# Optimization experiments

Hardware: AMD Instinct MI355X
Metric: run time of the kernel (lower is better)

The kernel has to match this reference:

```python
import jax, jax.numpy as jnp
import numpy as np

B, S, D, H, E, K = 4, 2048, 1024, 2048, 8, 2


def setup_inputs() -> dict:
    key = jax.random.key(0)
    ks = jax.random.split(key, 5)
    x = jax.random.normal(ks[0], (B, S, D), dtype=jnp.float32)
    Wr = jax.random.normal(ks[1], (D, E), dtype=jnp.float32) * 0.02  # router weight
    w1 = jax.random.normal(ks[2], (E, D, H), dtype=jnp.float32) * 0.02  # gate proj per expert
    w3 = jax.random.normal(ks[3], (E, D, H), dtype=jnp.float32) * 0.02  # up proj per expert
    w2 = jax.random.normal(ks[4], (E, H, D), dtype=jnp.float32) * 0.02  # down proj per expert
    return {"x": x, "Wr": Wr, "w1": w1, "w2": w2, "w3": w3}


def reference(x, Wr, w1, w2, w3):
    b, s, d = x.shape
    e = Wr.shape[1]
    flat = x.reshape(b * s, d)                      # [T, D]
    logits = flat @ Wr                              # [T, E]
    probs = jax.nn.softmax(logits, axis=-1)
    vals, idx = jax.lax.top_k(probs, K)             # [T, K]
    weights = vals / jnp.sum(vals, axis=-1, keepdims=True)
    onehot = jax.nn.one_hot(idx, e, dtype=flat.dtype)   # [T, K, E]
    cw = jnp.einsum('tke,tk->te', onehot, weights)      # combine weight per (token, expert)

    # naive dense: every expert computes every token, masked by combine weights
    out = jnp.zeros_like(flat)
    for ei in range(e):  # fixed small structural loop over experts
        h = jax.nn.silu(flat @ w1[ei]) * (flat @ w3[ei])   # [T, H]
        out = out + (h @ w2[ei]) * cw[:, ei:ei + 1]

    # aux load-balancing loss (usage uses any() over top-k slots, as in torch code)
    usage = (onehot.sum(axis=1) > 0).astype(flat.dtype).mean(axis=0)  # [E]
    prob_mass = probs.mean(axis=0)                                     # [E]
    aux_loss = e * jnp.sum(usage * prob_mass)
    return out.reshape(b, s, d), aux_loss
```

## Files before the change

kernel.cpp:

```cpp
#include <hip/hip_runtime.h>
#include <hip/hip_bf16.h>
#include <cstdint>
#include <cstddef>

#define T_TOK 8192
#define DIM   1024
#define HID   2048
#define NE    8
#define CAP   2816

typedef __attribute__((ext_vector_type(8))) short bf16x8;
typedef __attribute__((ext_vector_type(4))) float f32x4;
using bf16 = __hip_bfloat16;

__device__ __forceinline__ void gload16(const bf16* g, bf16* l) {
    __builtin_amdgcn_global_load_lds(
        (const __attribute__((address_space(1))) unsigned int*)(g),
        (__attribute__((address_space(3))) unsigned int*)(l), 16, 0, 0);
}
__device__ __forceinline__ float b2f(unsigned short u) {
    return __uint_as_float(((unsigned int)u) << 16);
}
#define MFMA16(a, b, c) __builtin_amdgcn_mfma_f32_16x16x32_bf16((a), (b), (c), 0, 0, 0)
#define BARRIER() asm volatile("s_barrier" ::: "memory")
#define WAITVM3() asm volatile("s_waitcnt vmcnt(3)" ::: "memory")
#define WAITVM0() asm volatile("s_waitcnt vmcnt(0)" ::: "memory")

__global__ __launch_bounds__(256) void k_transpose_all(const float* __restrict__ w1,
                                                       const float* __restrict__ w3,
                                                       const float* __restrict__ w2,
                                                       bf16* __restrict__ w1t,
                                                       bf16* __restrict__ w3t,
                                                       bf16* __restrict__ w2t) {
    __shared__ float tile[64][65];
    int z = blockIdx.z;
    const float* in = (z == 0) ? w1 : (z == 1) ? w3 : w2;
    bf16* out = (z == 0) ? w1t : (z == 1) ? w3t : w2t;
    int R = (z == 2) ? HID : DIM;
    int C = (z == 2) ? DIM : HID;
    int e = blockIdx.y;
    int ct = C >> 6;
    int r0 = (blockIdx.x / ct) << 6;
    int c0 = (blockIdx.x % ct) << 6;
    const float* src = in + (size_t)e * R * C;
    bf16* dst = out + (size_t)e * R * C;
    int s = threadIdx.x & 15, g = threadIdx.x >> 4;
#pragma unroll
    for (int j = 0; j < 4; ++j) {
        int row = j * 16 + g;
        float4 v = *(const float4*)(src + (size_t)(r0 + row) * C + c0 + s * 4);
        tile[row][s * 4 + 0] = v.x; tile[row][s * 4 + 1] = v.y;
        tile[row][s * 4 + 2] = v.z; tile[row][s * 4 + 3] = v.w;
    }
    __syncthreads();
#pragma unroll
    for (int j = 0; j < 4; ++j) {
        int c = j * 16 + g;
        int r = s * 4;
        bf16 o[4] = {__float2bfloat16(tile[r][c]),     __float2bfloat16(tile[r + 1][c]),
                     __float2bfloat16(tile[r + 2][c]), __float2bfloat16(tile[r + 3][c])};
        *(uint2*)(dst + (size_t)(c0 + c) * R + r0 + r) = *(const uint2*)o;
    }
}

__global__ __launch_bounds__(256) void k_logits(const float* __restrict__ x,
                                                const float* __restrict__ Wr,
                                                float* __restrict__ logits,
                                                bf16* __restrict__ xb) {
    __shared__ float wl[NE][DIM];
    for (int o = threadIdx.x; o < NE * DIM; o += 256) {
        int e = o >> 10, d = o & (DIM - 1);
        wl[e][d] = Wr[d * NE + e];
    }
    __syncthreads();
    int wid = threadIdx.x >> 6, lane = threadIdx.x & 63;
    int t = blockIdx.x * 4 + wid;
    const float* xr = x + (size_t)t * DIM;
    double acc[NE];
#pragma unroll
    for (int e = 0; e < NE; ++e) acc[e] = 0.0;
#pragma unroll
    for (int i = 0; i < DIM / 256; ++i) {
        int base = i * 256 + lane * 4;
        float4 v = *(const float4*)(xr + base);
        bf16 o[4] = {__float2bfloat16(v.x), __float2bfloat16(v.y),
                     __float2bfloat16(v.z), __float2bfloat16(v.w)};
        *(uint2*)(xb + (size_t)t * DIM + base) = *(const uint2*)o;
#pragma unroll
        for (int e = 0; e < NE; ++e)
            acc[e] += (double)v.x * wl[e][base] + (double)v.y * wl[e][base + 1]
                    + (double)v.z * wl[e][base + 2] + (double)v.w * wl[e][base + 3];
    }
#pragma unroll
    for (int e = 0; e < NE; ++e) {
        double v = acc[e];
        for (int m = 32; m >= 1; m >>= 1) v += __shfl_xor(v, m);
        if (lane == 0) logits[t * NE + e] = (float)v;
    }
}

__global__ __launch_bounds__(256) void k_route(const float* __restrict__ logits,
                                               int* counts, int* seg_tok, float* seg_w,
                                               int* slotpos, float* probsum) {
    int t = blockIdx.x * 256 + threadIdx.x;
    float l[NE];
#pragma unroll
    for (int e = 0; e < NE; ++e) l[e] = logits[t * NE + e];
    float mx = l[0];
#pragma unroll
    for (int e = 1; e < NE; ++e) mx = fmaxf(mx, l[e]);
    float p[NE], s = 0.f;
#pragma unroll
    for (int e = 0; e < NE; ++e) { p[e] = expf(l[e] - mx); s += p[e]; }
    float inv = 1.f / s;
#pragma unroll
    for (int e = 0; e < NE; ++e) p[e] *= inv;
    int e0 = 0; float v0 = p[0];
#pragma unroll
    for (int e = 1; e < NE; ++e) if (p[e] > v0) { v0 = p[e]; e0 = e; }
    int e1 = -1; float v1 = -1.f;
#pragma unroll
    for (int e = 0; e < NE; ++e) if (e != e0 && p[e] > v1) { v1 = p[e]; e1 = e; }
    float wsum = v0 + v1;
    float w0 = v0 / wsum, w1 = v1 / wsum;

    int lane = threadIdx.x & 63, wid = threadIdx.x >> 6;
    __shared__ float ps[4][NE];
#pragma unroll
    for (int e = 0; e < NE; ++e) {
        float v = p[e];
        for (int m = 32; m >= 1; m >>= 1) v += __shfl_xor(v, m);
        if (lane == 0) ps[wid][e] = v;
    }
    __syncthreads();
    if (threadIdx.x < NE) {
        float v = ps[0][threadIdx.x] + ps[1][threadIdx.x] + ps[2][threadIdx.x] + ps[3][threadIdx.x];
        atomicAdd(&probsum[threadIdx.x], v);
    }
    for (int slot = 0; slot < 2; ++slot) {
        int   e  = slot ? e1 : e0;
        float wv = slot ? w1 : w0;
#pragma unroll
        for (int ex = 0; ex < NE; ++ex) {
            unsigned long long m = __ballot(e == ex);
            if (e == ex) {
                int leader = __ffsll(m) - 1;
                int base = 0;
                if (lane == leader) base = atomicAdd(&counts[ex], __popcll(m));
                base = __shfl(base, leader);
                int pos = base + (int)__popcll(m & ((1ull << lane) - 1ull));
                if (pos < CAP) {
                    seg_tok[ex * CAP + pos] = t;
                    seg_w[ex * CAP + pos]  = wv;
                    slotpos[2 * t + slot]  = ex * CAP + pos;
                } else {
                    slotpos[2 * t + slot]  = -1;
                }
            }
        }
    }
}

__global__ __launch_bounds__(512, 2) void k_gemm1(const bf16* __restrict__ xb,
                                                  const bf16* __restrict__ w1t,
                                                  const bf16* __restrict__ w3t,
                                                  const int* __restrict__ counts,
                                                  const int* __restrict__ seg_tok,
                                                  bf16* __restrict__ h) {
    __shared__ __align__(16) bf16 lds[24576];
    __shared__ int toks[128];
    const int NTL = HID / 128;
    int flat = blockIdx.y * gridDim.x + blockIdx.x;
    int cpx  = (gridDim.x * NE) >> 3;
    int swz  = (flat & 7) * cpx + (flat >> 3);
    int e    = swz / gridDim.x;
    int tile = swz % gridDim.x;
    int mtile = tile / NTL, ntile = tile % NTL;
    int cnt = counts[e]; if (cnt > CAP) cnt = CAP;
    if (mtile * 128 >= cnt) return;

    int tx = threadIdx.x, lane = tx & 63, wid = tx >> 6;
    if (tx < 128) {
        int slot = mtile * 128 + tx;
        toks[tx] = seg_tok[e * CAP + (slot < cnt ? slot : 0)];
    }
    __syncthreads();

    int srow = tx >> 2;
    int sc8  = (((tx & 3) ^ ((tx >> 3) & 3)) << 3);
    const bf16* sA  = xb  + (size_t)toks[srow] * DIM + sc8;
    const bf16* sBg = w1t + ((size_t)e * HID + ntile * 128 + srow) * DIM + sc8;
    const bf16* sBu = w3t + ((size_t)e * HID + ntile * 128 + srow) * DIM + sc8;

    int l15 = lane & 15, lh = lane >> 4;
    int role = wid >> 2, pp = wid & 3, rh = pp >> 1, ch = pp & 1;
    int ach = ((lh ^ ((l15 >> 1) & 3)) << 3);
    const int rAoff = (rh * 64 + l15) * 32 + ach;
    const int rBoff = 4096 + role * 4096 + (ch * 64 + l15) * 32 + ach;

    f32x4 acc[4][4];
    f32x4 zero4 = {0.f, 0.f, 0.f, 0.f};
#pragma unroll
    for (int m = 0; m < 4; ++m)
#pragma unroll
        for (int n = 0; n < 4; ++n) acc[m][n] = zero4;

#define G1_STAGE(s, ko) do { \
        gload16(sA  + (ko), lds + (s) * 12288 + tx * 8); \
        gload16(sBg + (ko), lds + (s) * 12288 + 4096 + tx * 8); \
        gload16(sBu + (ko), lds + (s) * 12288 + 8192 + tx * 8); } while (0)

    G1_STAGE(0, 0);
    const int NT = DIM / 32;
#pragma unroll 1
    for (int k = 0; k < NT; ++k) {
        if (k + 1 < NT) G1_STAGE((k + 1) & 1, (k + 1) * 32);
        if (k < NT - 1) WAITVM3(); else WAITVM0();
        BARRIER();
        const bf16* base = lds + (k & 1) * 12288;
        bf16x8 a0 = *(const bf16x8*)(base + rAoff);
        bf16x8 a1 = *(const bf16x8*)(base + rAoff + 512);
        bf16x8 a2 = *(const bf16x8*)(base + rAoff + 1024);
        bf16x8 a3 = *(const bf16x8*)(base + rAoff + 1536);
        bf16x8 b0 = *(const bf16x8*)(base + rBoff);
        bf16x8 b1 = *(const bf16x8*)(base + rBoff + 512);
        bf16x8 b2 = *(const bf16x8*)(base + rBoff + 1024);
        bf16x8 b3 = *(const bf16x8*)(base + rBoff + 1536);
        __builtin_amdgcn_s_setprio(1);
        acc[0][0] = MFMA16(a0, b0, acc[0][0]); acc[1][0] = MFMA16(a1, b0, acc[1][0]);
        acc[2][0] = MFMA16(a2, b0, acc[2][0]); acc[3][0] = MFMA16(a3, b0, acc[3][0]);
        acc[0][1] = MFMA16(a0, b1, acc[0][1]); acc[1][1] = MFMA16(a1, b1, acc[1][1]);
        acc[2][1] = MFMA16(a2, b1, acc[2][1]); acc[3][1] = MFMA16(a3, b1, acc[3][1]);
        acc[0][2] = MFMA16(a0, b2, acc[0][2]); acc[1][2] = MFMA16(a1, b2, acc[1][2]);
        acc[2][2] = MFMA16(a2, b2, acc[2][2]); acc[3][2] = MFMA16(a3, b2, acc[3][2]);
        acc[0][3] = MFMA16(a0, b3, acc[0][3]); acc[1][3] = MFMA16(a1, b3, acc[1][3]);
        acc[2][3] = MFMA16(a2, b3, acc[2][3]); acc[3][3] = MFMA16(a3, b3, acc[3][3]);
        __builtin_amdgcn_s_setprio(0);
        BARRIER();
    }
#undef G1_STAGE

    if (role == 1) {
#pragma unroll
        for (int m = 0; m < 4; ++m)
#pragma unroll
            for (int n = 0; n < 4; ++n)
#pragma unroll
                for (int r = 0; r < 4; ++r) {
                    int row = rh * 64 + m * 16 + lh * 4 + r;
                    int col = ch * 64 + n * 16 + l15;
                    lds[row * 128 + col] = __float2bfloat16(acc[m][n][r]);
                }
    }
    BARRIER();
    if (role == 0) {
        bf16* hdst = h + ((size_t)e * CAP + (size_t)mtile * 128) * HID + ntile * 128;
#pragma unroll
        for (int m = 0; m < 4; ++m)
#pragma unroll
            for (int n = 0; n < 4; ++n)
#pragma unroll
                for (int r = 0; r < 4; ++r) {
                    int row = rh * 64 + m * 16 + lh * 4 + r;
                    int col = ch * 64 + n * 16 + l15;
                    float gg = acc[m][n][r];
                    float uu = b2f(*(const unsigned short*)&lds[row * 128 + col]);
                    float hv = gg / (1.f + __expf(-gg)) * uu;
                    hdst[(size_t)row * HID + col] = __float2bfloat16(hv);
                }
    }
}

__global__ __launch_bounds__(512, 2) void k_gemm2(const bf16* __restrict__ hbuf,
                                                  const bf16* __restrict__ w2t,
                                                  const int* __restrict__ counts,
                                                  const float* __restrict__ seg_w,
                                                  bf16* __restrict__ ybuf) {
    __shared__ __align__(16) bf16 lds[24576];
    __shared__ float wts[128];
    const int NTL = DIM / 256;
    int flat = blockIdx.y * gridDim.x + blockIdx.x;
    int cpx  = (gridDim.x * NE) >> 3;
    int swz  = (flat & 7) * cpx + (flat >> 3);
    int e    = swz / gridDim.x;
    int tile = swz % gridDim.x;
    int mtile = tile / NTL, ntile = tile % NTL;
    int cnt = counts[e]; if (cnt > CAP) cnt = CAP;
    if (mtile * 128 >= cnt) return;

    int tx = threadIdx.x, lane = tx & 63, wid = tx >> 6;
    if (tx < 128) {
        int slot = mtile * 128 + tx;
        wts[tx] = (slot < cnt) ? seg_w[e * CAP + slot] : 0.f;
    }
    __syncthreads();

    int srow = tx >> 2;
    int sc8  = (((tx & 3) ^ ((tx >> 3) & 3)) << 3);
    const bf16* sA  = hbuf + ((size_t)e * CAP + mtile * 128 + srow) * HID + sc8;
    const bf16* sB0 = w2t + ((size_t)e * DIM + ntile * 256 + srow) * HID + sc8;
    const bf16* sB1 = w2t + ((size_t)e * DIM + ntile * 256 + 128 + srow) * HID + sc8;

    int l15 = lane & 15, lh = lane >> 4;
    int rh = wid >> 2, cq = wid & 3;
    int ach = ((lh ^ ((l15 >> 1) & 3)) << 3);
    const int rAoff = (rh * 64 + l15) * 32 + ach;
    const int rBoff = 4096 + (cq * 64 + l15) * 32 + ach;

    f32x4 acc[4][4];
    f32x4 zero4 = {0.f, 0.f, 0.f, 0.f};
#pragma unroll
    for (int m = 0; m < 4; ++m)
#pragma unroll
        for (int n = 0; n < 4; ++n) acc[m][n] = zero4;

#define G2_STAGE(s, ko) do { \
        gload16(sA  + (ko), lds + (s) * 12288 + tx * 8); \
        gload16(sB0 + (ko), lds + (s) * 12288 + 4096 + tx * 8); \
        gload16(sB1 + (ko), lds + (s) * 12288 + 8192 + tx * 8); } while (0)

    G2_STAGE(0, 0);
    const int NT = HID / 32;
#pragma unroll 1
    for (int k = 0; k < NT; ++k) {
        if (k + 1 < NT) G2_STAGE((k + 1) & 1, (k + 1) * 32);
        if (k < NT - 1) WAITVM3(); else WAITVM0();
        BARRIER();
        const bf16* base = lds + (k & 1) * 12288;
        bf16x8 a0 = *(const bf16x8*)(base + rAoff);
        bf16x8 a1 = *(const bf16x8*)(base + rAoff + 512);
        bf16x8 a2 = *(const bf16x8*)(base + rAoff + 1024);
        bf16x8 a3 = *(const bf16x8*)(base + rAoff + 1536);
        bf16x8 b0 = *(const bf16x8*)(base + rBoff);
        bf16x8 b1 = *(const bf16x8*)(base + rBoff + 512);
        bf16x8 b2 = *(const bf16x8*)(base + rBoff + 1024);
        bf16x8 b3 = *(const bf16x8*)(base + rBoff + 1536);
        __builtin_amdgcn_s_setprio(1);
        acc[0][0] = MFMA16(a0, b0, acc[0][0]); acc[1][0] = MFMA16(a1, b0, acc[1][0]);
        acc[2][0] = MFMA16(a2, b0, acc[2][0]); acc[3][0] = MFMA16(a3, b0, acc[3][0]);
        acc[0][1] = MFMA16(a0, b1, acc[0][1]); acc[1][1] = MFMA16(a1, b1, acc[1][1]);
        acc[2][1] = MFMA16(a2, b1, acc[2][1]); acc[3][1] = MFMA16(a3, b1, acc[3][1]);
        acc[0][2] = MFMA16(a0, b2, acc[0][2]); acc[1][2] = MFMA16(a1, b2, acc[1][2]);
        acc[2][2] = MFMA16(a2, b2, acc[2][2]); acc[3][2] = MFMA16(a3, b2, acc[3][2]);
        acc[0][3] = MFMA16(a0, b3, acc[0][3]); acc[1][3] = MFMA16(a1, b3, acc[1][3]);
        acc[2][3] = MFMA16(a2, b3, acc[2][3]); acc[3][3] = MFMA16(a3, b3, acc[3][3]);
        __builtin_amdgcn_s_setprio(0);
        BARRIER();
    }
#undef G2_STAGE

    bf16* ydst = ybuf + ((size_t)e * CAP + (size_t)mtile * 128) * DIM + ntile * 256;
#pragma unroll
    for (int m = 0; m < 4; ++m)
#pragma unroll
        for (int n = 0; n < 4; ++n)
#pragma unroll
            for (int r = 0; r < 4; ++r) {
                int row = rh * 64 + m * 16 + lh * 4 + r;
                int col = cq * 64 + n * 16 + l15;
                ydst[(size_t)row * DIM + col] = __float2bfloat16(acc[m][n][r] * wts[row]);
            }
}

__global__ __launch_bounds__(256) void k_combine(const bf16* __restrict__ yb,
                                                 const int* __restrict__ slotpos,
                                                 float* __restrict__ out) {
    int t = blockIdx.x;
    int s0 = slotpos[2 * t], s1 = slotpos[2 * t + 1];
    int d = threadIdx.x * 4;
    float4 a = {0.f, 0.f, 0.f, 0.f};
    if (s0 >= 0) {
        ushort4 v = *(const ushort4*)(yb + (size_t)s0 * DIM + d);
        a.x += b2f(v.x); a.y += b2f(v.y); a.z += b2f(v.z); a.w += b2f(v.w);
    }
    if (s1 >= 0) {
        ushort4 v = *(const ushort4*)(yb + (size_t)s1 * DIM + d);
        a.x += b2f(v.x); a.y += b2f(v.y); a.z += b2f(v.z); a.w += b2f(v.w);
    }
    *(float4*)(out + (size_t)t * DIM + d) = a;
}

__global__ void k_aux(const int* __restrict__ counts, const float* __restrict__ probsum,
                      float* __restrict__ outaux) {
    if (threadIdx.x == 0 && blockIdx.x == 0) {
        float s = 0.f;
        for (int e = 0; e < NE; ++e)
            s += ((float)counts[e] / (float)T_TOK) * (probsum[e] / (float)T_TOK);
        *outaux = (float)NE * s;
    }
}

extern "C" void kernel_launch(void* const* d_in, const int* in_sizes, int n_in,
                              void* d_out, int out_size, void* d_ws, size_t ws_size,
                              hipStream_t stream) {
    const float* x  = (const float*)d_in[0];
    const float* Wr = (const float*)d_in[1];
    const float* w1 = (const float*)d_in[2];
    const float* w2 = (const float*)d_in[3];
    const float* w3 = (const float*)d_in[4];
    float* out = (float*)d_out;

    char* ws = (char*)d_ws;
    size_t off = 0;
    auto alloc = [&](size_t bytes) { void* p = ws + off; off += (bytes + 255) & ~(size_t)255; return p; };
    bf16*  xb      = (bf16*)alloc((size_t)T_TOK * DIM * 2);
    bf16*  w1t     = (bf16*)alloc((size_t)NE * HID * DIM * 2);
    bf16*  w3t     = (bf16*)alloc((size_t)NE * HID * DIM * 2);
    bf16*  w2t     = (bf16*)alloc((size_t)NE * DIM * HID * 2);
    bf16*  hbuf    = (bf16*)alloc((size_t)NE * CAP * HID * 2);
    float* logits  = (float*)alloc((size_t)T_TOK * NE * 4);
    int*   counts  = (int*)alloc(256);
    int*   segtok  = (int*)alloc((size_t)NE * CAP * 4);
    float* segw    = (float*)alloc((size_t)NE * CAP * 4);
    int*   slotpos = (int*)alloc((size_t)T_TOK * 2 * 4);
    float* probsum = (float*)alloc(256);
    bf16*  ybuf    = w1t;
    (void)ws_size; (void)in_sizes; (void)n_in;

    hipMemsetAsync(counts, 0, 256, stream);
    hipMemsetAsync(probsum, 0, 256, stream);

    k_logits<<<T_TOK / 4, 256, 0, stream>>>(x, Wr, logits, xb);
    k_route<<<T_TOK / 256, 256, 0, stream>>>(logits, counts, segtok, segw, slotpos, probsum);

    dim3 gt((DIM / 64) * (HID / 64), NE, 3);
    k_transpose_all<<<gt, 256, 0, stream>>>(w1, w3, w2, w1t, w3t, w2t);

    dim3 g1((CAP / 128) * (HID / 128), NE);
    k_gemm1<<<g1, 512, 0, stream>>>(xb, w1t, w3t, counts, segtok, hbuf);
    dim3 g2((CAP / 128) * (DIM / 256), NE);
    k_gemm2<<<g2, 512, 0, stream>>>(hbuf, w2t, counts, segw, ybuf);

    k_combine<<<T_TOK, 256, 0, stream>>>(ybuf, slotpos, out);
    k_aux<<<1, 64, 0, stream>>>(counts, probsum, out + (size_t)T_TOK * DIM);
}
```

Measured before the change: 427.6 us.

## Enlarge expert GEMM tiles to 256 rows with K=64 stages and interleaved prefetch

Both expert GEMM kernels now use 256-row M tiles and 64-wide K steps, with each wave holding an 8x4 grid of 16x16 accumulators, so every LDS fragment feeds more MFMAs. Global-to-LDS loads are double-buffered two stages ahead and issued between MFMA quads, with barrier and lgkmcnt waits that pin the schedule. LDS grows to 128KB per block, which together with the larger accumulator set cuts occupancy. Fewer blocks are launched, which worsens tail waste when an expert's token count is not a multiple of 256.

```diff
diff --git a/kernel.cpp b/kernel.cpp
--- a/kernel.cpp
+++ b/kernel.cpp
@@ -22,9 +22,46 @@
     return __uint_as_float(((unsigned int)u) << 16);
 }
 #define MFMA16(a, b, c) __builtin_amdgcn_mfma_f32_16x16x32_bf16((a), (b), (c), 0, 0, 0)
-#define BARRIER() asm volatile("s_barrier" ::: "memory")
-#define WAITVM3() asm volatile("s_waitcnt vmcnt(3)" ::: "memory")
-#define WAITVM0() asm volatile("s_waitcnt vmcnt(0)" ::: "memory")
+#define BARRIER()  asm volatile("s_barrier" ::: "memory")
+#define WAITVM8()  asm volatile("s_waitcnt vmcnt(8)" ::: "memory")
+#define WAITVM0()  asm volatile("s_waitcnt vmcnt(0)" ::: "memory")
+#define LGKM0SB()  do { asm volatile("s_waitcnt lgkmcnt(0)" ::: "memory"); \
+                        __builtin_amdgcn_sched_barrier(0); } while (0)
+
+#define QUAD(MB, NB) do { \
+    __builtin_amdgcn_s_setprio(1); \
+    acc[(MB)+0][(NB)+0] = MFMA16(af[0][0], bfr[(NB)+0][0], acc[(MB)+0][(NB)+0]); \
+    acc[(MB)+1][(NB)+0] = MFMA16(af[1][0], bfr[(NB)+0][0], acc[(MB)+1][(NB)+0]); \
+    acc[(MB)+2][(NB)+0] = MFMA16(af[2][0], bfr[(NB)+0][0], acc[(MB)+2][(NB)+0]); \
+    acc[(MB)+3][(NB)+0] = MFMA16(af[3][0], bfr[(NB)+0][0], acc[(MB)+3][(NB)+0]); \
+    acc[(MB)+0][(NB)+1] = MFMA16(af[0][0], bfr[(NB)+1][0], acc[(MB)+0][(NB)+1]); \
+    acc[(MB)+1][(NB)+1] = MFMA16(af[1][0], bfr[(NB)+1][0], acc[(MB)+1][(NB)+1]); \
+    acc[(MB)+2][(NB)+1] = MFMA16(af[2][0], bfr[(NB)+1][0], acc[(MB)+2][(NB)+1]); \
+    acc[(MB)+3][(NB)+1] = MFMA16(af[3][0], bfr[(NB)+1][0], acc[(MB)+3][(NB)+1]); \
+    acc[(MB)+0][(NB)+0] = MFMA16(af[0][1], bfr[(NB)+0][1], acc[(MB)+0][(NB)+0]); \
+    acc[(MB)+1][(NB)+0] = MFMA16(af[1][1], bfr[(NB)+0][1], acc[(MB)+1][(NB)+0]); \
+    acc[(MB)+2][(NB)+0] = MFMA16(af[2][1], bfr[(NB)+0][1], acc[(MB)+2][(NB)+0]); \
+    acc[(MB)+3][(NB)+0] = MFMA16(af[3][1], bfr[(NB)+0][1], acc[(MB)+3][(NB)+0]); \
+    acc[(MB)+0][(NB)+1] = MFMA16(af[0][1], bfr[(NB)+1][1], acc[(MB)+0][(NB)+1]); \
+    acc[(MB)+1][(NB)+1] = MFMA16(af[1][1], bfr[(NB)+1][1], acc[(MB)+1][(NB)+1]); \
+    acc[(MB)+2][(NB)+1] = MFMA16(af[2][1], bfr[(NB)+1][1], acc[(MB)+2][(NB)+1]); \
+    acc[(MB)+3][(NB)+1] = MFMA16(af[3][1], bfr[(NB)+1][1], acc[(MB)+3][(NB)+1]); \
+    __builtin_amdgcn_s_setprio(0); } while (0)
+
+#define RD_A4(mb) do { \
+    af[0][0] = *(const bf16x8*)(Ab + ((mb)+0)*1024 + c0sw); \
+    af[0][1] = *(const bf16x8*)(Ab + ((mb)+0)*1024 + c1sw); \
+    af[1][0] = *(const bf16x8*)(Ab + ((mb)+1)*1024 + c0sw); \
+    af[1][1] = *(const bf16x8*)(Ab + ((mb)+1)*1024 + c1sw); \
+    af[2][0] = *(const bf16x8*)(Ab + ((mb)+2)*1024 + c0sw); \
+    af[2][1] = *(const bf16x8*)(Ab + ((mb)+2)*1024 + c1sw); \
+    af[3][0] = *(const bf16x8*)(Ab + ((mb)+3)*1024 + c0sw); \
+    af[3][1] = *(const bf16x8*)(Ab + ((mb)+3)*1024 + c1sw); } while (0)
+#define RD_B2(nb) do { \
+    bfr[(nb)+0][0] = *(const bf16x8*)(Bb + ((nb)+0)*1024 + c0sw); \
+    bfr[(nb)+0][1] = *(const bf16x8*)(Bb + ((nb)+0)*1024 + c1sw); \
+    bfr[(nb)+1][0] = *(const bf16x8*)(Bb + ((nb)+1)*1024 + c0sw); \
+    bfr[(nb)+1][1] = *(const bf16x8*)(Bb + ((nb)+1)*1024 + c1sw); } while (0)
 
 __global__ __launch_bounds__(256) void k_transpose_all(const float* __restrict__ w1,
                                                        const float* __restrict__ w3,
@@ -167,8 +204,8 @@
                                                   const int* __restrict__ counts,
                                                   const int* __restrict__ seg_tok,
                                                   bf16* __restrict__ h) {
-    __shared__ __align__(16) bf16 lds[24576];
-    __shared__ int toks[128];
+    __shared__ __align__(16) bf16 lds[65536];
+    __shared__ int toks[256];
     const int NTL = HID / 128;
     int flat = blockIdx.y * gridDim.x + blockIdx.x;
     int cpx  = (gridDim.x * NE) >> 3;
@@ -177,94 +214,112 @@
     int tile = swz % gridDim.x;
     int mtile = tile / NTL, ntile = tile % NTL;
     int cnt = counts[e]; if (cnt > CAP) cnt = CAP;
-    if (mtile * 128 >= cnt) return;
+    if (mtile * 256 >= cnt) return;
 
     int tx = threadIdx.x, lane = tx & 63, wid = tx >> 6;
-    if (tx < 128) {
-        int slot = mtile * 128 + tx;
-        toks[tx] = seg_tok[e * CAP + (slot < cnt ? slot : 0)];
+    for (int i = tx; i < 256; i += 512) {
+        int slot = mtile * 256 + i;
+        toks[i] = seg_tok[e * CAP + (slot < cnt ? slot : 0)];
     }
     __syncthreads();
 
-    int srow = tx >> 2;
-    int sc8  = (((tx & 3) ^ ((tx >> 3) & 3)) << 3);
-    const bf16* sA  = xb  + (size_t)toks[srow] * DIM + sc8;
-    const bf16* sBg = w1t + ((size_t)e * HID + ntile * 128 + srow) * DIM + sc8;
-    const bf16* sBu = w3t + ((size_t)e * HID + ntile * 128 + srow) * DIM + sc8;
+    int srl = tx >> 3;
+    int sch = (((tx & 7) ^ (srl & 7)) << 3);
+    const bf16* tA[2][2];
+#pragma unroll
+    for (int ah = 0; ah < 2; ++ah)
+#pragma unroll
+        for (int r = 0; r < 2; ++r)
+            tA[ah][r] = xb + (size_t)toks[ah * 128 + r * 64 + srl] * DIM + sch;
+    const bf16* sBg = w1t + ((size_t)e * HID + ntile * 128 + srl) * DIM + sch;
+    const bf16* sBu = w3t + ((size_t)e * HID + ntile * 128 + srl) * DIM + sch;
+    bf16* dD = lds + tx * 8;
 
     int l15 = lane & 15, lh = lane >> 4;
-    int role = wid >> 2, pp = wid & 3, rh = pp >> 1, ch = pp & 1;
-    int ach = ((lh ^ ((l15 >> 1) & 3)) << 3);
-    const int rAoff = (rh * 64 + l15) * 32 + ach;
-    const int rBoff = 4096 + role * 4096 + (ch * 64 + l15) * 32 + ach;
-
-    f32x4 acc[4][4];
+    int wm = wid >> 2, wn = wid & 3, hn = wn >> 1, ns = wn & 1;
+    int c0sw = ((lh ^ (l15 & 7)) << 3);
+    int c1sw = (((4 + lh) ^ (l15 & 7)) << 3);
+
+    f32x4 acc[8][4];
     f32x4 zero4 = {0.f, 0.f, 0.f, 0.f};
 #pragma unroll
-    for (int m = 0; m < 4; ++m)
+    for (int m = 0; m < 8; ++m)
 #pragma unroll
         for (int n = 0; n < 4; ++n) acc[m][n] = zero4;
 
-#define G1_STAGE(s, ko) do { \
-        gload16(sA  + (ko), lds + (s) * 12288 + tx * 8); \
-        gload16(sBg + (ko), lds + (s) * 12288 + 4096 + tx * 8); \
-        gload16(sBu + (ko), lds + (s) * 12288 + 8192 + tx * 8); } while (0)
-
-    G1_STAGE(0, 0);
-    const int NT = DIM / 32;
+#define STG_A1(bo, ah, ko) do { \
+        gload16(tA[ah][0] + (ko), dD + (bo) + (ah) * 8192); \
+        gload16(tA[ah][1] + (ko), dD + (bo) + (ah) * 8192 + 4096); } while (0)
+#define STG_Bg1(bo, ko) do { \
+        gload16(sBg + (ko),                      dD + (bo) + 16384); \
+        gload16(sBg + (size_t)64 * DIM + (ko),   dD + (bo) + 16384 + 4096); } while (0)
+#define STG_Bu1(bo, ko) do { \
+        gload16(sBu + (ko),                      dD + (bo) + 24576); \
+        gload16(sBu + (size_t)64 * DIM + (ko),   dD + (bo) + 24576 + 4096); } while (0)
+
+    STG_A1(0, 0, 0); STG_A1(0, 1, 0); STG_Bg1(0, 0); STG_Bu1(0, 0);
+    STG_A1(32768, 0, 64); STG_A1(32768, 1, 64); STG_Bg1(32768, 64); STG_Bu1(32768, 64);
+    WAITVM8();
+    BARRIER();
+
+    const int NT = DIM / 64;
 #pragma unroll 1
-    for (int k = 0; k < NT; ++k) {
-        if (k + 1 < NT) G1_STAGE((k + 1) & 1, (k + 1) * 32);
-        if (k < NT - 1) WAITVM3(); else WAITVM0();
-        BARRIER();
-        const bf16* base = lds + (k & 1) * 12288;
-        bf16x8 a0 = *(const bf16x8*)(base + rAoff);
-        bf16x8 a1 = *(const bf16x8*)(base + rAoff + 512);
-        bf16x8 a2 = *(const bf16x8*)(base + rAoff + 1024);
-        bf16x8 a3 = *(const bf16x8*)(base + rAoff + 1536);
-        bf16x8 b0 = *(const bf16x8*)(base + rBoff);
-        bf16x8 b1 = *(const bf16x8*)(base + rBoff + 512);
-        bf16x8 b2 = *(const bf16x8*)(base + rBoff + 1024);
-        bf16x8 b3 = *(const bf16x8*)(base + rBoff + 1536);
-        __builtin_amdgcn_s_setprio(1);
-        acc[0][0] = MFMA16(a0, b0, acc[0][0]); acc[1][0] = MFMA16(a1, b0, acc[1][0]);
-        acc[2][0] = MFMA16(a2, b0, acc[2][0]); acc[3][0] = MFMA16(a3, b0, acc[3][0]);
-        acc[0][1] = MFMA16(a0, b1, acc[0][1]); acc[1][1] = MFMA16(a1, b1, acc[1][1]);
-        acc[2][1] = MFMA16(a2, b1, acc[2][1]); acc[3][1] = MFMA16(a3, b1, acc[3][1]);
-        acc[0][2] = MFMA16(a0, b2, acc[0][2]); acc[1][2] = MFMA16(a1, b2, acc[1][2]);
-        acc[2][2] = MFMA16(a2, b2, acc[2][2]); acc[3][2] = MFMA16(a3, b2, acc[3][2]);
-        acc[0][3] = MFMA16(a0, b3, acc[0][3]); acc[1][3] = MFMA16(a1, b3, acc[1][3]);
-        acc[2][3] = MFMA16(a2, b3, acc[2][3]); acc[3][3] = MFMA16(a3, b3, acc[3][3]);
-        __builtin_amdgcn_s_setprio(0);
-        BARRIER();
-    }
-#undef G1_STAGE
-
-    if (role == 1) {
-#pragma unroll
-        for (int m = 0; m < 4; ++m)
+    for (int t = 0; t < NT; ++t) {
+        const int bo = (t & 1) << 15;
+        const int ko2 = (t + 2) << 6;
+        const bool st = (t + 2 < NT);
+        const bf16* Ab = lds + bo + wm * 8192 + l15 * 64;
+        const bf16* Bb = lds + bo + 16384 + hn * 8192 + ns * 4096 + l15 * 64;
+        bf16x8 af[4][2], bfr[4][2];
+        RD_A4(0); RD_B2(0);
+        BARRIER(); LGKM0SB();
+        QUAD(0, 0);
+        BARRIER();
+        RD_B2(2);
+        BARRIER(); LGKM0SB();
+        QUAD(0, 2);
+        BARRIER();
+        RD_A4(4);
+        if (st) { STG_Bg1(bo, ko2); STG_Bu1(bo, ko2); }
+        BARRIER(); LGKM0SB();
+        QUAD(4, 0);
+        BARRIER();
+        if (st) { STG_A1(bo, 0, ko2); STG_A1(bo, 1, ko2); }
+        BARRIER();
+        QUAD(4, 2);
+        if (st) WAITVM8(); else WAITVM0();
+        BARRIER();
+    }
+#undef STG_A1
+#undef STG_Bg1
+#undef STG_Bu1
+
+    if (hn == 1) {
+#pragma unroll
+        for (int m = 0; m < 8; ++m)
 #pragma unroll
             for (int n = 0; n < 4; ++n)
 #pragma unroll
                 for (int r = 0; r < 4; ++r) {
-                    int row = rh * 64 + m * 16 + lh * 4 + r;
-                    int col = ch * 64 + n * 16 + l15;
-                    lds[row * 128 + col] = __float2bfloat16(acc[m][n][r]);
+                    int row = m * 16 + lh * 4 + r;
+                    int col = n * 16 + l15;
+                    lds[((ns * 2 + wm) * 128 + row) * 64 + col] = __float2bfloat16(acc[m][n][r]);
                 }
     }
-    BARRIER();
-    if (role == 0) {
-        bf16* hdst = h + ((size_t)e * CAP + (size_t)mtile * 128) * HID + ntile * 128;
-#pragma unroll
-        for (int m = 0; m < 4; ++m)
+    __syncthreads();
+    if (hn == 0) {
+        bf16* hdst = h + ((size_t)e * CAP + (size_t)mtile * 256 + wm * 128) * HID
+                       + ntile * 128 + ns * 64;
+#pragma unroll
+        for (int m = 0; m < 8; ++m)
 #pragma unroll
             for (int n = 0; n < 4; ++n)
 #pragma unroll
                 for (int r = 0; r < 4; ++r) {
-                    int row = rh * 64 + m * 16 + lh * 4 + r;
-                    int col = ch * 64 + n * 16 + l15;
+                    int row = m * 16 + lh * 4 + r;
+                    int col = n * 16 + l15;
                     float gg = acc[m][n][r];
-                    float uu = b2f(*(const unsigned short*)&lds[row * 128 + col]);
+                    float uu = b2f(*(const unsigned short*)&lds[((ns * 2 + wm) * 128 + row) * 64 + col]);
                     float hv = gg / (1.f + __expf(-gg)) * uu;
                     hdst[(size_t)row * HID + col] = __float2bfloat16(hv);
                 }
@@ -276,8 +331,8 @@
                                                   const int* __restrict__ counts,
                                                   const float* __restrict__ seg_w,
                                                   bf16* __restrict__ ybuf) {
-    __shared__ __align__(16) bf16 lds[24576];
-    __shared__ float wts[128];
+    __shared__ __align__(16) bf16 lds[65536];
+    __shared__ float wts[256];
     const int NTL = DIM / 256;
     int flat = blockIdx.y * gridDim.x + blockIdx.x;
     int cpx  = (gridDim.x * NE) >> 3;
@@ -286,79 +341,88 @@
     int tile = swz % gridDim.x;
     int mtile = tile / NTL, ntile = tile % NTL;
     int cnt = counts[e]; if (cnt > CAP) cnt = CAP;
-    if (mtile * 128 >= cnt) return;
+    if (mtile * 256 >= cnt) return;
 
     int tx = threadIdx.x, lane = tx & 63, wid = tx >> 6;
-    if (tx < 128) {
-        int slot = mtile * 128 + tx;
-        wts[tx] = (slot < cnt) ? seg_w[e * CAP + slot] : 0.f;
+    for (int i = tx; i < 256; i += 512) {
+        int slot = mtile * 256 + i;
+        wts[i] = (slot < cnt) ? seg_w[e * CAP + slot] : 0.f;
     }
     __syncthreads();
 
-    int srow = tx >> 2;
-    int sc8  = (((tx & 3) ^ ((tx >> 3) & 3)) << 3);
-    const bf16* sA  = hbuf + ((size_t)e * CAP + mtile * 128 + srow) * HID + sc8;
-    const bf16* sB0 = w2t + ((size_t)e * DIM + ntile * 256 + srow) * HID + sc8;
-    const bf16* sB1 = w2t + ((size_t)e * DIM + ntile * 256 + 128 + srow) * HID + sc8;
+    int srl = tx >> 3;
+    int sch = (((tx & 7) ^ (srl & 7)) << 3);
+    const bf16* sA = hbuf + ((size_t)e * CAP + mtile * 256 + srl) * HID + sch;
+    const bf16* sB = w2t  + ((size_t)e * DIM + ntile * 256 + srl) * HID + sch;
+    bf16* dD = lds + tx * 8;
 
     int l15 = lane & 15, lh = lane >> 4;
-    int rh = wid >> 2, cq = wid & 3;
-    int ach = ((lh ^ ((l15 >> 1) & 3)) << 3);
-    const int rAoff = (rh * 64 + l15) * 32 + ach;
-    const int rBoff = 4096 + (cq * 64 + l15) * 32 + ach;
-
-    f32x4 acc[4][4];
+    int wm = wid >> 2, wn = wid & 3, hn = wn >> 1, ns = wn & 1;
+    int c0sw = ((lh ^ (l15 & 7)) << 3);
+    int c1sw = (((4 + lh) ^ (l15 & 7)) << 3);
+
+    f32x4 acc[8][4];
     f32x4 zero4 = {0.f, 0.f, 0.f, 0.f};
 #pragma unroll
-    for (int m = 0; m < 4; ++m)
+    for (int m = 0; m < 8; ++m)
 #pragma unroll
         for (int n = 0; n < 4; ++n) acc[m][n] = zero4;
 
-#define G2_STAGE(s, ko) do { \
-        gload16(sA  + (ko), lds + (s) * 12288 + tx * 8); \
-        gload16(sB0 + (ko), lds + (s) * 12288 + 4096 + tx * 8); \
-        gload16(sB1 + (ko), lds + (s) * 12288 + 8192 + tx * 8); } while (0)
-
-    G2_STAGE(0, 0);
-    const int NT = HID / 32;
+#define STG_A2(bo, ah, ko) do { \
+        gload16(sA + (size_t)((ah) * 128     ) * HID + (ko), dD + (bo) + (ah) * 8192); \
+        gload16(sA + (size_t)((ah) * 128 + 64) * HID + (ko), dD + (bo) + (ah) * 8192 + 4096); } while (0)
+#define STG_B2(bo, bh, ko) do { \
+        gload16(sB + (size_t)((bh) * 128     ) * HID + (ko), dD + (bo) + 16384 + (bh) * 8192); \
+        gload16(sB + (size_t)((bh) * 128 + 64) * HID + (ko), dD + (bo) + 16384 + (bh) * 8192 + 4096); } while (0)
+
+    STG_A2(0, 0, 0); STG_A2(0, 1, 0); STG_B2(0, 0, 0); STG_B2(0, 1, 0);
+    STG_A2(32768, 0, 64); STG_A2(32768, 1, 64); STG_B2(32768, 0, 64); STG_B2(32768, 1, 64);
+    WAITVM8();
+    BARRIER();
+
+    const int NT = HID / 64;
 #pragma unroll 1
-    for (int k = 0; k < NT; ++k) {
-        if (k + 1 < NT) G2_STAGE((k + 1) & 1, (k + 1) * 32);
-        if (k < NT - 1) WAITVM3(); else WAITVM0();
-        BARRIER();
-        const bf16* base = lds + (k & 1) * 12288;
-        bf16x8 a0 = *(const bf16x8*)(base + rAoff);
-        bf16x8 a1 = *(const bf16x8*)(base + rAoff + 512);
-        bf16x8 a2 = *(const bf16x8*)(base + rAoff + 1024);
-        bf16x8 a3 = *(const bf16x8*)(base + rAoff + 1536);
-        bf16x8 b0 = *(const bf16x8*)(base + rBoff);
-        bf16x8 b1 = *(const bf16x8*)(base + rBoff + 512);
-        bf16x8 b2 = *(const bf16x8*)(base + rBoff + 1024);
-        bf16x8 b3 = *(const bf16x8*)(base + rBoff + 1536);
-        __builtin_amdgcn_s_setprio(1);
-        acc[0][0] = MFMA16(a0, b0, acc[0][0]); acc[1][0] = MFMA16(a1, b0, acc[1][0]);
-        acc[2][0] = MFMA16(a2, b0, acc[2][0]); acc[3][0] = MFMA16(a3, b0, acc[3][0]);
-        acc[0][1] = MFMA16(a0, b1, acc[0][1]); acc[1][1] = MFMA16(a1, b1, acc[1][1]);
-        acc[2][1] = MFMA16(a2, b1, acc[2][1]); acc[3][1] = MFMA16(a3, b1, acc[3][1]);
-        acc[0][2] = MFMA16(a0, b2, acc[0][2]); acc[1][2] = MFMA16(a1, b2, acc[1][2]);
-        acc[2][2] = MFMA16(a2, b2, acc[2][2]); acc[3][2] = MFMA16(a3, b2, acc[3][2]);
-        acc[0][3] = MFMA16(a0, b3, acc[0][3]); acc[1][3] = MFMA16(a1, b3, acc[1][3]);
-        acc[2][3] = MFMA16(a2, b3, acc[2][3]); acc[3][3] = MFMA16(a3, b3, acc[3][3]);
-        __builtin_amdgcn_s_setprio(0);
-        BARRIER();
-    }
-#undef G2_STAGE
-
-    bf16* ydst = ybuf + ((size_t)e * CAP + (size_t)mtile * 128) * DIM + ntile * 256;
-#pragma unroll
-    for (int m = 0; m < 4; ++m)
+    for (int t = 0; t < NT; ++t) {
+        const int bo = (t & 1) << 15;
+        const int ko2 = (t + 2) << 6;
+        const bool st = (t + 2 < NT);
+        const bf16* Ab = lds + bo + wm * 8192 + l15 * 64;
+        const bf16* Bb = lds + bo + 16384 + hn * 8192 + ns * 4096 + l15 * 64;
+        bf16x8 af[4][2], bfr[4][2];
+        RD_A4(0); RD_B2(0);
+        BARRIER(); LGKM0SB();
+        QUAD(0, 0);
+        BARRIER();
+        RD_B2(2);
+        BARRIER(); LGKM0SB();
+        QUAD(0, 2);
+        BARRIER();
+        RD_A4(4);
+        if (st) { STG_B2(bo, 0, ko2); STG_B2(bo, 1, ko2); }
+        BARRIER(); LGKM0SB();
+        QUAD(4, 0);
+        BARRIER();
+        if (st) { STG_A2(bo, 0, ko2); STG_A2(bo, 1, ko2); }
+        BARRIER();
+        QUAD(4, 2);
+        if (st) WAITVM8(); else WAITVM0();
+        BARRIER();
+    }
+#undef STG_A2
+#undef STG_B2
+
+    bf16* ydst = ybuf + ((size_t)e * CAP + (size_t)mtile * 256 + wm * 128) * DIM
+                      + ntile * 256 + wn * 64;
+#pragma unroll
+    for (int m = 0; m < 8; ++m)
 #pragma unroll
         for (int n = 0; n < 4; ++n)
 #pragma unroll
             for (int r = 0; r < 4; ++r) {
-                int row = rh * 64 + m * 16 + lh * 4 + r;
-                int col = cq * 64 + n * 16 + l15;
-                ydst[(size_t)row * DIM + col] = __float2bfloat16(acc[m][n][r] * wts[row]);
+                int row = m * 16 + lh * 4 + r;
+                int col = n * 16 + l15;
+                ydst[(size_t)row * DIM + col] =
+                    __float2bfloat16(acc[m][n][r] * wts[wm * 128 + row]);
             }
 }
 
@@ -426,9 +490,9 @@
     dim3 gt((DIM / 64) * (HID / 64), NE, 3);
     k_transpose_all<<<gt, 256, 0, stream>>>(w1, w3, w2, w1t, w3t, w2t);
 
-    dim3 g1((CAP / 128) * (HID / 128), NE);
+    dim3 g1((CAP / 256) * (HID / 128), NE);
     k_gemm1<<<g1, 512, 0, stream>>>(xb, w1t, w3t, counts, segtok, hbuf);
-    dim3 g2((CAP / 128) * (DIM / 256), NE);
+    dim3 g2((CAP / 256) * (DIM / 256), NE);
     k_gemm2<<<g2, 512, 0, stream>>>(hbuf, w2t, counts, segw, ybuf);
 
     k_combine<<<T_TOK, 256, 0, stream>>>(ybuf, slotpos, out);
```

Result: slower. 470.0 us (+9.9%).
